# Performance work log

Measured on AMD Instinct MI355X. Metric: run time of the kernel, lower is better.

Reference implementation:

```python
import jax, jax.numpy as jnp
import numpy as np

BS, C, H, W = 64, 3, 512, 512
DROP_PIX = 0.3          # fraction of pixels dropped
NOISE_STD = 0.1         # gaussian multiplicative noise std
RNG_SEED = 42           # internal forward randomness (torch RNG analog)


def setup_inputs() -> dict:
    key = jax.random.key(0)
    x = jax.random.normal(key, (BS, C, H, W), dtype=jnp.float32)
    return {"x": x}


def reference(x):
    bs, c, h, w = x.shape
    hw = h * w
    len_keep = int(hw * (1.0 - DROP_PIX))
    k_mask, k_noise = jax.random.split(jax.random.key(RNG_SEED))

    # Per-sample random permutation of pixel indices, keep first len_keep.
    # argsort of iid uniforms == uniformly random permutation (all bs at once,
    # replacing the Python loop + per-iteration randperm of the original).
    u = jax.random.uniform(k_mask, (bs, hw))
    keep_idx = jnp.argsort(u, axis=1)[:, :len_keep]          # [bs, len_keep]
    mask = jnp.zeros((bs, hw), dtype=x.dtype)
    mask = mask.at[jnp.arange(bs)[:, None], keep_idx].set(1.0)
    mask = mask.reshape(bs, 1, h, w)

    # drop_type == 'zeros'
    x = x * mask

    # additive_noise: gaussian multiplicative noise (real-valued branch)
    noise = jax.random.normal(k_noise, x.shape, dtype=x.dtype) * NOISE_STD + 1.0
    x = x * noise
    return x, mask
```

## Files before the change

### kernel.cpp

```cpp
#include <hip/hip_runtime.h>
#include <hip/hip_bf16.h>

typedef unsigned int u32;
typedef unsigned long long u64;

__host__ __device__ __forceinline__ void tf2x32(u32 k0, u32 k1, u32 x0, u32 x1,
                                                u32& o0, u32& o1)
{
    const u32 ks2 = k0 ^ k1 ^ 0x1BD11BDAu;
    x0 += k0; x1 += k1;
#define TF_R(r) { x0 += x1; x1 = (x1 << (r)) | (x1 >> (32 - (r))); x1 ^= x0; }
    TF_R(13) TF_R(15) TF_R(26) TF_R(6)
    x0 += k1; x1 += ks2 + 1u;
    TF_R(17) TF_R(29) TF_R(16) TF_R(24)
    x0 += ks2; x1 += k0 + 2u;
    TF_R(13) TF_R(15) TF_R(26) TF_R(6)
    x0 += k0; x1 += k1 + 3u;
    TF_R(17) TF_R(29) TF_R(16) TF_R(24)
    x0 += k1; x1 += ks2 + 4u;
    TF_R(13) TF_R(15) TF_R(26) TF_R(6)
    x0 += ks2; x1 += k0 + 5u;
#undef TF_R
    o0 = x0; o1 = x1;
}

__device__ __forceinline__ u32 rbits(u32 k0, u32 k1, u32 e)
{
    u32 o0, o1; tf2x32(k0, k1, 0u, e, o0, o1); return o0 ^ o1;
}

#define HW        262144u
#define PMASK     262143u
#define KEEP      183500u
#define NX        50331648u
#define NM        16777216u
#define LO_F      (-0.99999994039535522461f)

__device__ __forceinline__ float noise_from_bits(u32 bits)
{
    float f  = __uint_as_float((bits >> 9) | 0x3F800000u) - 1.0f;
    float un = fmaf(f, 2.0f, LO_F);
    un = fmaxf(LO_F, un);
    float w = -__logf(fmaf(-un, un, 1.0f));
    float p;
    if (w < 5.0f) {
        w -= 2.5f;
        p = 2.81022636e-08f;
        p = fmaf(p, w, 3.43273939e-07f);
        p = fmaf(p, w, -3.5233877e-06f);
        p = fmaf(p, w, -4.39150654e-06f);
        p = fmaf(p, w, 0.00021858087f);
        p = fmaf(p, w, -0.00125372503f);
        p = fmaf(p, w, -0.00417768164f);
        p = fmaf(p, w, 0.246640727f);
        p = fmaf(p, w, 1.50140941f);
    } else {
        w = __fsqrt_rn(w) - 3.0f;
        p = -0.000200214257f;
        p = fmaf(p, w, 0.000100950558f);
        p = fmaf(p, w, 0.00134934322f);
        p = fmaf(p, w, -0.00367342844f);
        p = fmaf(p, w, 0.00573950773f);
        p = fmaf(p, w, -0.0076224613f);
        p = fmaf(p, w, 0.00943887047f);
        p = fmaf(p, w, 1.00167406f);
        p = fmaf(p, w, 2.83297682f);
    }
    float ei = p * un;
    return fmaf(1.41421356f * ei, 0.1f, 1.0f);
}

__global__ __launch_bounds__(256) void k1_gen_hist(u32 mk0, u32 mk1, u32* mbuf, u32* hist)
{
    __shared__ u32 lh[4096];
    const int t = threadIdx.x;
    const u32 blk = blockIdx.x;
    const u32 row = blk >> 4;
    const u32 base = blk << 14;
#pragma unroll
    for (int i = 0; i < 16; ++i) lh[t + (i << 8)] = 0;
    __syncthreads();
    uint4* mv = (uint4*)mbuf;
#pragma unroll 1
    for (int i = 0; i < 16; ++i) {
        u32 vi = (u32)(i << 8) + (u32)t;
        u32 e = base + (vi << 2);
        uint4 q;
        q.x = rbits(mk0, mk1, e)     >> 9;
        q.y = rbits(mk0, mk1, e + 1) >> 9;
        q.z = rbits(mk0, mk1, e + 2) >> 9;
        q.w = rbits(mk0, mk1, e + 3) >> 9;
        mv[(base >> 2) + vi] = q;
        atomicAdd(&lh[q.x >> 11], 1u);
        atomicAdd(&lh[q.y >> 11], 1u);
        atomicAdd(&lh[q.z >> 11], 1u);
        atomicAdd(&lh[q.w >> 11], 1u);
    }
    __syncthreads();
    u32* gh = hist + (row << 12);
#pragma unroll
    for (int i = 0; i < 16; ++i) {
        u32 idx = (u32)t + (i << 8);
        u32 v = lh[idx];
        if (v) atomicAdd(&gh[idx], v);
    }
}

template <int PER>
__device__ __forceinline__ void rank_scan(const u32* h, u32 k, u32* sh, u32& bin, u32& rem)
{
    const int t = threadIdx.x;
    u32 v[PER]; u32 s = 0;
#pragma unroll
    for (int i = 0; i < PER; ++i) { v[i] = h[t * PER + i]; s += v[i]; }
    sh[t] = s;
    __syncthreads();
    if (t == 0) {
        u32 run = 0; u32 c = 0;
        for (; c < 255u; ++c) { u32 cs = sh[c]; if (run + cs >= k) break; run += cs; }
        sh[256] = c; sh[257] = run;
    }
    __syncthreads();
    u32 c = sh[256];
    if (t == (int)c) {
        u32 run = sh[257];
        u32 b = (u32)t * PER + PER - 1; u32 r = k - run;
#pragma unroll
        for (int i = 0; i < PER; ++i) {
            if (run + v[i] >= k) { b = (u32)t * PER + i; r = k - run; break; }
            run += v[i];
        }
        sh[256] = b; sh[257] = r;
    }
    __syncthreads();
    bin = sh[256]; rem = sh[257];
    __syncthreads();
}

__global__ __launch_bounds__(256) void k2b_finehist(const u32* mbuf, const u32* hist,
                                                    u32* fhist, u32* rowBr)
{
    __shared__ u32 sh[258];
    __shared__ u32 fh[2048];
    const int t = threadIdx.x;
    const u32 blk = blockIdx.x;
    const u32 row = blk >> 4;
    u32 B, r;
    rank_scan<16>(hist + (row << 12), KEEP, sh, B, r);
    if ((blk & 15u) == 0 && t == 0) { rowBr[row * 2] = B; rowBr[row * 2 + 1] = r; }
#pragma unroll
    for (int i = 0; i < 8; ++i) fh[t + (i << 8)] = 0;
    __syncthreads();
    const uint4* mv = (const uint4*)mbuf + (blk << 12);
#pragma unroll 1
    for (int i = 0; i < 16; ++i) {
        uint4 q = mv[(i << 8) + t];
        if ((q.x >> 11) == B) atomicAdd(&fh[q.x & 2047u], 1u);
        if ((q.y >> 11) == B) atomicAdd(&fh[q.y & 2047u], 1u);
        if ((q.z >> 11) == B) atomicAdd(&fh[q.z & 2047u], 1u);
        if ((q.w >> 11) == B) atomicAdd(&fh[q.w & 2047u], 1u);
    }
    __syncthreads();
    u32* gf = fhist + (row << 11);
#pragma unroll
    for (int i = 0; i < 8; ++i) {
        u32 idx = (u32)t + (i << 8);
        u32 v = fh[idx];
        if (v) atomicAdd(&gf[idx], v);
    }
}

__global__ __launch_bounds__(256) void k2d_ties(const u32* mbuf, const u32* fhist,
                                                const u32* rowBr, u32* rowM,
                                                u32* tiecnt, u32* tielist)
{
    __shared__ u32 sh[258];
    const int t = threadIdx.x;
    const u32 blk = blockIdx.x;
    const u32 row = blk >> 4;
    u32 r = rowBr[row * 2 + 1];
    u32 B = rowBr[row * 2];
    u32 f, r2;
    rank_scan<8>(fhist + (row << 11), r, sh, f, r2);
    u32 mstar = (B << 11) | f;
    if ((blk & 15u) == 0 && t == 0) { rowM[row * 2] = mstar; rowM[row * 2 + 1] = r2; }
    const uint4* mv = (const uint4*)mbuf + (blk << 12);
#pragma unroll 1
    for (int i = 0; i < 16; ++i) {
        u32 vi = (u32)(i << 8) + (u32)t;
        uint4 q = mv[vi];
        u32 p = ((blk & 15u) << 14) + (vi << 2);
        if (q.x == mstar) { u32 pos = atomicAdd(&tiecnt[row], 1u); if (pos < 256u) tielist[(row << 8) + pos] = p; }
        if (q.y == mstar) { u32 pos = atomicAdd(&tiecnt[row], 1u); if (pos < 256u) tielist[(row << 8) + pos] = p + 1; }
        if (q.z == mstar) { u32 pos = atomicAdd(&tiecnt[row], 1u); if (pos < 256u) tielist[(row << 8) + pos] = p + 2; }
        if (q.w == mstar) { u32 pos = atomicAdd(&tiecnt[row], 1u); if (pos < 256u) tielist[(row << 8) + pos] = p + 3; }
    }
}

__global__ __launch_bounds__(64) void k2e_select(const u32* rowM, const u32* tiecnt,
                                                 const u32* tielist, u64* rowsel)
{
    __shared__ u32 list[256];
    const int t = threadIdx.x;
    const u32 row = blockIdx.x;
    u32 mstar = rowM[row * 2], r2 = rowM[row * 2 + 1];
    u32 cnt = tiecnt[row]; if (cnt > 256u) cnt = 256u;
    for (u32 i = (u32)t; i < cnt; i += 64u) list[i] = tielist[(row << 8) + i];
    __syncthreads();
    if (t == 0) {
        if (r2 > cnt) r2 = cnt;
        u32 pstar = 0;
        for (u32 it = 0; it < r2; ++it) {
            u32 mn = 0xFFFFFFFFu, mi = 0;
            for (u32 i2 = 0; i2 < cnt; ++i2) if (list[i2] < mn) { mn = list[i2]; mi = i2; }
            pstar = mn; list[mi] = 0xFFFFFFFFu;
        }
        rowsel[row] = ((u64)mstar << 18) | (u64)pstar;
    }
}

__global__ __launch_bounds__(256) void k3_mask(u32* mbuf, const u64* rowsel)
{
    u32 tid = blockIdx.x * 256u + threadIdx.x;
    u32 row = tid >> 16;
    u64 kst = rowsel[row];
    uint4 q = ((const uint4*)mbuf)[tid];
    u32 p = (tid << 2) & PMASK;
    float4 o;
    o.x = ((((u64)q.x << 18) | (u64)(p))     <= kst) ? 1.0f : 0.0f;
    o.y = ((((u64)q.y << 18) | (u64)(p + 1)) <= kst) ? 1.0f : 0.0f;
    o.z = ((((u64)q.z << 18) | (u64)(p + 2)) <= kst) ? 1.0f : 0.0f;
    o.w = ((((u64)q.w << 18) | (u64)(p + 3)) <= kst) ? 1.0f : 0.0f;
    ((float4*)mbuf)[tid] = o;
}

__global__ __launch_bounds__(256) void k4_final(const float4* x4, const float* maskf,
                                                float4* out4, u32 nk0, u32 nk1)
{
    u32 tid = blockIdx.x * 256u + threadIdx.x;
    u32 e = tid << 2;
    u32 b = e / 786432u;
    u32 p = e & PMASK;
    float4 mk = *(const float4*)(maskf + ((b << 18) | p));
    float4 xv = x4[tid];
    float4 r;
    r.x = (xv.x * mk.x) * noise_from_bits(rbits(nk0, nk1, e));
    r.y = (xv.y * mk.y) * noise_from_bits(rbits(nk0, nk1, e + 1));
    r.z = (xv.z * mk.z) * noise_from_bits(rbits(nk0, nk1, e + 2));
    r.w = (xv.w * mk.w) * noise_from_bits(rbits(nk0, nk1, e + 3));
    out4[tid] = r;
}

extern "C" void kernel_launch(void* const* d_in, const int* in_sizes, int n_in,
                              void* d_out, int out_size, void* d_ws, size_t ws_size,
                              hipStream_t stream) {
    const float* x = (const float*)d_in[0];
    float* xout = (float*)d_out;
    u32*  outu = (u32*)d_out;
    u32*  mbuf = (u32*)(xout + NX);

    u32* hist    = outu;
    u32* fhist   = outu + 262144;
    u32* tiecnt  = outu + 393216;
    u32* tielist = outu + 393472;
    u32* rowBr   = outu + 409856;
    u32* rowM    = outu + 410112;
    u64* rowsel  = (u64*)(outu + 410368);

    u32 mk0, mk1, nk0, nk1;
    tf2x32(0u, 42u, 0u, 0u, mk0, mk1);
    tf2x32(0u, 42u, 0u, 1u, nk0, nk1);

    hipMemsetAsync(hist, 0, (262144u + 131072u + 64u) * sizeof(u32), stream);
    k1_gen_hist<<<1024, 256, 0, stream>>>(mk0, mk1, mbuf, hist);
    k2b_finehist<<<1024, 256, 0, stream>>>(mbuf, hist, fhist, rowBr);
    k2d_ties<<<1024, 256, 0, stream>>>(mbuf, fhist, rowBr, rowM, tiecnt, tielist);
    k2e_select<<<64, 64, 0, stream>>>(rowM, tiecnt, tielist, rowsel);
    k3_mask<<<16384, 256, 0, stream>>>(mbuf, rowsel);
    k4_final<<<49152, 256, 0, stream>>>((const float4*)x, (const float*)mbuf,
                                        (float4*)xout, nk0, nk1);
    (void)d_ws; (void)ws_size; (void)in_sizes; (void)n_in; (void)out_size;
}
```

Measured before the change: 514.2 us.

## Replace multi-pass radix select with windowed candidate select and fused mask/noise kernel

The exact multi-pass histogram selection over a stored 64MB key buffer is replaced by a single pass. That pass regenerates the random keys, counts keys below a fixed window near the expected 70% quantile, and collects only in-window candidates per row. A single small kernel per row then finds the exact threshold from those candidates. The final kernel recomputes the mask keys from the RNG and produces the mask and all three noisy channels in one pass. This removes most global memory traffic and several launches, at the cost of hashing the mask keys twice and relying on the threshold statistically falling inside the window (candidate capacity caps).

```diff
diff --git a/kernel.cpp b/kernel.cpp
--- a/kernel.cpp
+++ b/kernel.cpp
@@ -1,8 +1,8 @@
 #include <hip/hip_runtime.h>
-#include <hip/hip_bf16.h>
 
 typedef unsigned int u32;
 typedef unsigned long long u64;
+typedef unsigned char u8;
 
 __host__ __device__ __forceinline__ void tf2x32(u32 k0, u32 k1, u32 x0, u32 x1,
                                                 u32& o0, u32& o1)
@@ -35,6 +35,19 @@
 #define NX        50331648u
 #define NM        16777216u
 #define LO_F      (-0.99999994039535522461f)
+
+#define WLO       5806464u
+#define WWIDTH    131072u
+#define NBIN      4096
+#define ROWCAP    6144
+#define BLKCAP    512
+
+#define CAND_B    (64u * ROWCAP * 8u)
+#define WS_BYTES  (CAND_B + 512u + 512u)
+
+__device__ u64 g_cand[64 * ROWCAP];
+__device__ u64 g_rowsel[64];
+__device__ u32 g_cnts[128];
 
 __device__ __forceinline__ float noise_from_bits(u32 bits)
 {
@@ -70,185 +83,156 @@
     return fmaf(1.41421356f * ei, 0.1f, 1.0f);
 }
 
-__global__ __launch_bounds__(256) void k1_gen_hist(u32 mk0, u32 mk1, u32* mbuf, u32* hist)
-{
-    __shared__ u32 lh[4096];
+__global__ __launch_bounds__(256) void k1_scan(u32 mk0, u32 mk1,
+                                               u32* __restrict__ cnts,
+                                               u64* __restrict__ cand)
+{
+    __shared__ u64 s_cand[BLKCAP];
+    __shared__ u32 s_cnt, s_below, s_base;
     const int t = threadIdx.x;
     const u32 blk = blockIdx.x;
     const u32 row = blk >> 4;
     const u32 base = blk << 14;
-#pragma unroll
-    for (int i = 0; i < 16; ++i) lh[t + (i << 8)] = 0;
-    __syncthreads();
-    uint4* mv = (uint4*)mbuf;
+    if (t == 0) { s_cnt = 0; s_below = 0; }
+    __syncthreads();
+    u32 below = 0;
 #pragma unroll 1
     for (int i = 0; i < 16; ++i) {
         u32 vi = (u32)(i << 8) + (u32)t;
         u32 e = base + (vi << 2);
-        uint4 q;
-        q.x = rbits(mk0, mk1, e)     >> 9;
-        q.y = rbits(mk0, mk1, e + 1) >> 9;
-        q.z = rbits(mk0, mk1, e + 2) >> 9;
-        q.w = rbits(mk0, mk1, e + 3) >> 9;
-        mv[(base >> 2) + vi] = q;
-        atomicAdd(&lh[q.x >> 11], 1u);
-        atomicAdd(&lh[q.y >> 11], 1u);
-        atomicAdd(&lh[q.z >> 11], 1u);
-        atomicAdd(&lh[q.w >> 11], 1u);
-    }
-    __syncthreads();
-    u32* gh = hist + (row << 12);
-#pragma unroll
-    for (int i = 0; i < 16; ++i) {
-        u32 idx = (u32)t + (i << 8);
-        u32 v = lh[idx];
-        if (v) atomicAdd(&gh[idx], v);
-    }
-}
-
-template <int PER>
-__device__ __forceinline__ void rank_scan(const u32* h, u32 k, u32* sh, u32& bin, u32& rem)
-{
+#pragma unroll
+        for (int j = 0; j < 4; ++j) {
+            u32 m = rbits(mk0, mk1, e + (u32)j) >> 9;
+            below += (m < WLO) ? 1u : 0u;
+            if (m - WLO < WWIDTH) {
+                u32 p = ((blk & 15u) << 14) + (vi << 2) + (u32)j;
+                u32 pos = atomicAdd(&s_cnt, 1u);
+                if (pos < BLKCAP) s_cand[pos] = ((u64)m << 18) | (u64)p;
+            }
+        }
+    }
+    atomicAdd(&s_below, below);
+    __syncthreads();
+    u32 cnt = s_cnt; if (cnt > BLKCAP) cnt = BLKCAP;
+    if (t == 0) {
+        atomicAdd(&cnts[row], s_below);
+        s_base = atomicAdd(&cnts[64 + row], cnt);
+    }
+    __syncthreads();
+    u32 gbase = s_base;
+    for (u32 i = (u32)t; i < cnt; i += 256u) {
+        u32 gi = gbase + i;
+        if (gi < ROWCAP) cand[row * ROWCAP + gi] = s_cand[i];
+    }
+}
+
+__global__ __launch_bounds__(256) void k2_select(u32* __restrict__ cnts,
+                                                 const u64* __restrict__ cand,
+                                                 u64* __restrict__ rowsel)
+{
+    __shared__ u32 h[NBIN];
+    __shared__ u32 sh[258];
+    __shared__ u64 tie[64];
+    __shared__ u32 tiecnt;
     const int t = threadIdx.x;
-    u32 v[PER]; u32 s = 0;
-#pragma unroll
-    for (int i = 0; i < PER; ++i) { v[i] = h[t * PER + i]; s += v[i]; }
+    const u32 row = blockIdx.x;
+    u32 n = cnts[64 + row]; if (n > ROWCAP) n = ROWCAP;
+    u32 below = cnts[row];
+    u32 r = KEEP - below;
+#pragma unroll
+    for (int i = 0; i < NBIN / 256; ++i) h[t + (i << 8)] = 0;
+    if (t == 0) tiecnt = 0;
+    __syncthreads();
+    const u64* rc = cand + row * ROWCAP;
+    for (u32 i = (u32)t; i < n; i += 256u) {
+        u32 m = (u32)(rc[i] >> 18);
+        atomicAdd(&h[(m - WLO) >> 5], 1u);
+    }
+    __syncthreads();
+    u32 v[16]; u32 s = 0;
+#pragma unroll
+    for (int i = 0; i < 16; ++i) { v[i] = h[t * 16 + i]; s += v[i]; }
     sh[t] = s;
     __syncthreads();
     if (t == 0) {
         u32 run = 0; u32 c = 0;
-        for (; c < 255u; ++c) { u32 cs = sh[c]; if (run + cs >= k) break; run += cs; }
+        for (; c < 255u; ++c) { u32 cs = sh[c]; if (run + cs >= r) break; run += cs; }
         sh[256] = c; sh[257] = run;
     }
     __syncthreads();
     u32 c = sh[256];
     if (t == (int)c) {
         u32 run = sh[257];
-        u32 b = (u32)t * PER + PER - 1; u32 r = k - run;
-#pragma unroll
-        for (int i = 0; i < PER; ++i) {
-            if (run + v[i] >= k) { b = (u32)t * PER + i; r = k - run; break; }
+        u32 b = (u32)t * 16u + 15u; u32 r2 = r - run;
+#pragma unroll
+        for (int i = 0; i < 16; ++i) {
+            if (run + v[i] >= r) { b = (u32)t * 16u + (u32)i; r2 = r - run; break; }
             run += v[i];
         }
-        sh[256] = b; sh[257] = r;
-    }
-    __syncthreads();
-    bin = sh[256]; rem = sh[257];
-    __syncthreads();
-}
-
-__global__ __launch_bounds__(256) void k2b_finehist(const u32* mbuf, const u32* hist,
-                                                    u32* fhist, u32* rowBr)
-{
-    __shared__ u32 sh[258];
-    __shared__ u32 fh[2048];
-    const int t = threadIdx.x;
-    const u32 blk = blockIdx.x;
-    const u32 row = blk >> 4;
-    u32 B, r;
-    rank_scan<16>(hist + (row << 12), KEEP, sh, B, r);
-    if ((blk & 15u) == 0 && t == 0) { rowBr[row * 2] = B; rowBr[row * 2 + 1] = r; }
-#pragma unroll
-    for (int i = 0; i < 8; ++i) fh[t + (i << 8)] = 0;
-    __syncthreads();
-    const uint4* mv = (const uint4*)mbuf + (blk << 12);
-#pragma unroll 1
-    for (int i = 0; i < 16; ++i) {
-        uint4 q = mv[(i << 8) + t];
-        if ((q.x >> 11) == B) atomicAdd(&fh[q.x & 2047u], 1u);
-        if ((q.y >> 11) == B) atomicAdd(&fh[q.y & 2047u], 1u);
-        if ((q.z >> 11) == B) atomicAdd(&fh[q.z & 2047u], 1u);
-        if ((q.w >> 11) == B) atomicAdd(&fh[q.w & 2047u], 1u);
-    }
-    __syncthreads();
-    u32* gf = fhist + (row << 11);
-#pragma unroll
-    for (int i = 0; i < 8; ++i) {
-        u32 idx = (u32)t + (i << 8);
-        u32 v = fh[idx];
-        if (v) atomicAdd(&gf[idx], v);
-    }
-}
-
-__global__ __launch_bounds__(256) void k2d_ties(const u32* mbuf, const u32* fhist,
-                                                const u32* rowBr, u32* rowM,
-                                                u32* tiecnt, u32* tielist)
-{
-    __shared__ u32 sh[258];
-    const int t = threadIdx.x;
-    const u32 blk = blockIdx.x;
-    const u32 row = blk >> 4;
-    u32 r = rowBr[row * 2 + 1];
-    u32 B = rowBr[row * 2];
-    u32 f, r2;
-    rank_scan<8>(fhist + (row << 11), r, sh, f, r2);
-    u32 mstar = (B << 11) | f;
-    if ((blk & 15u) == 0 && t == 0) { rowM[row * 2] = mstar; rowM[row * 2 + 1] = r2; }
-    const uint4* mv = (const uint4*)mbuf + (blk << 12);
-#pragma unroll 1
-    for (int i = 0; i < 16; ++i) {
-        u32 vi = (u32)(i << 8) + (u32)t;
-        uint4 q = mv[vi];
-        u32 p = ((blk & 15u) << 14) + (vi << 2);
-        if (q.x == mstar) { u32 pos = atomicAdd(&tiecnt[row], 1u); if (pos < 256u) tielist[(row << 8) + pos] = p; }
-        if (q.y == mstar) { u32 pos = atomicAdd(&tiecnt[row], 1u); if (pos < 256u) tielist[(row << 8) + pos] = p + 1; }
-        if (q.z == mstar) { u32 pos = atomicAdd(&tiecnt[row], 1u); if (pos < 256u) tielist[(row << 8) + pos] = p + 2; }
-        if (q.w == mstar) { u32 pos = atomicAdd(&tiecnt[row], 1u); if (pos < 256u) tielist[(row << 8) + pos] = p + 3; }
-    }
-}
-
-__global__ __launch_bounds__(64) void k2e_select(const u32* rowM, const u32* tiecnt,
-                                                 const u32* tielist, u64* rowsel)
-{
-    __shared__ u32 list[256];
-    const int t = threadIdx.x;
-    const u32 row = blockIdx.x;
-    u32 mstar = rowM[row * 2], r2 = rowM[row * 2 + 1];
-    u32 cnt = tiecnt[row]; if (cnt > 256u) cnt = 256u;
-    for (u32 i = (u32)t; i < cnt; i += 64u) list[i] = tielist[(row << 8) + i];
+        sh[256] = b; sh[257] = r2;
+    }
+    __syncthreads();
+    u32 bstar = sh[256], r2 = sh[257];
+    u32 mlo = WLO + (bstar << 5), mhi = mlo + 32u;
+    for (u32 i = (u32)t; i < n; i += 256u) {
+        u64 k = rc[i];
+        u32 m = (u32)(k >> 18);
+        if (m >= mlo && m < mhi) {
+            u32 pos = atomicAdd(&tiecnt, 1u);
+            if (pos < 64u) tie[pos] = k;
+        }
+    }
     __syncthreads();
     if (t == 0) {
+        u32 cnt = tiecnt; if (cnt > 64u) cnt = 64u;
         if (r2 > cnt) r2 = cnt;
-        u32 pstar = 0;
+        u64 kst = 0;
         for (u32 it = 0; it < r2; ++it) {
-            u32 mn = 0xFFFFFFFFu, mi = 0;
-            for (u32 i2 = 0; i2 < cnt; ++i2) if (list[i2] < mn) { mn = list[i2]; mi = i2; }
-            pstar = mn; list[mi] = 0xFFFFFFFFu;
-        }
-        rowsel[row] = ((u64)mstar << 18) | (u64)pstar;
-    }
-}
-
-__global__ __launch_bounds__(256) void k3_mask(u32* mbuf, const u64* rowsel)
+            u64 mn = ~0ull; u32 mi = 0;
+            for (u32 i2 = 0; i2 < cnt; ++i2) if (tie[i2] < mn) { mn = tie[i2]; mi = i2; }
+            kst = mn; tie[mi] = ~0ull;
+        }
+        rowsel[row] = kst;
+        cnts[row] = 0;
+        cnts[64 + row] = 0;
+    }
+}
+
+__global__ __launch_bounds__(256) void k34_final(const float4* __restrict__ x4,
+                                                 float4* __restrict__ out4,
+                                                 float4* __restrict__ mask4,
+                                                 const u64* __restrict__ rowsel,
+                                                 u32 mk0, u32 mk1, u32 nk0, u32 nk1)
 {
     u32 tid = blockIdx.x * 256u + threadIdx.x;
     u32 row = tid >> 16;
     u64 kst = rowsel[row];
-    uint4 q = ((const uint4*)mbuf)[tid];
-    u32 p = (tid << 2) & PMASK;
-    float4 o;
-    o.x = ((((u64)q.x << 18) | (u64)(p))     <= kst) ? 1.0f : 0.0f;
-    o.y = ((((u64)q.y << 18) | (u64)(p + 1)) <= kst) ? 1.0f : 0.0f;
-    o.z = ((((u64)q.z << 18) | (u64)(p + 2)) <= kst) ? 1.0f : 0.0f;
-    o.w = ((((u64)q.w << 18) | (u64)(p + 3)) <= kst) ? 1.0f : 0.0f;
-    ((float4*)mbuf)[tid] = o;
-}
-
-__global__ __launch_bounds__(256) void k4_final(const float4* x4, const float* maskf,
-                                                float4* out4, u32 nk0, u32 nk1)
-{
-    u32 tid = blockIdx.x * 256u + threadIdx.x;
     u32 e = tid << 2;
-    u32 b = e / 786432u;
     u32 p = e & PMASK;
-    float4 mk = *(const float4*)(maskf + ((b << 18) | p));
-    float4 xv = x4[tid];
-    float4 r;
-    r.x = (xv.x * mk.x) * noise_from_bits(rbits(nk0, nk1, e));
-    r.y = (xv.y * mk.y) * noise_from_bits(rbits(nk0, nk1, e + 1));
-    r.z = (xv.z * mk.z) * noise_from_bits(rbits(nk0, nk1, e + 2));
-    r.w = (xv.w * mk.w) * noise_from_bits(rbits(nk0, nk1, e + 3));
-    out4[tid] = r;
+
+    u32 m0 = rbits(mk0, mk1, e)      >> 9;
+    u32 m1 = rbits(mk0, mk1, e + 1u) >> 9;
+    u32 m2 = rbits(mk0, mk1, e + 2u) >> 9;
+    u32 m3 = rbits(mk0, mk1, e + 3u) >> 9;
+    float4 mk;
+    mk.x = ((((u64)m0 << 18) | (u64)(p))      <= kst) ? 1.0f : 0.0f;
+    mk.y = ((((u64)m1 << 18) | (u64)(p + 1u)) <= kst) ? 1.0f : 0.0f;
+    mk.z = ((((u64)m2 << 18) | (u64)(p + 2u)) <= kst) ? 1.0f : 0.0f;
+    mk.w = ((((u64)m3 << 18) | (u64)(p + 3u)) <= kst) ? 1.0f : 0.0f;
+    mask4[tid] = mk;
+
+    u32 b3 = row * 3u;
+#pragma unroll
+    for (u32 cc = 0; cc < 3u; ++cc) {
+        u32 en = ((b3 + cc) << 18) | p;
+        float4 xv = x4[en >> 2];
+        float4 r;
+        r.x = (xv.x * mk.x) * noise_from_bits(rbits(nk0, nk1, en));
+        r.y = (xv.y * mk.y) * noise_from_bits(rbits(nk0, nk1, en + 1u));
+        r.z = (xv.z * mk.z) * noise_from_bits(rbits(nk0, nk1, en + 2u));
+        r.w = (xv.w * mk.w) * noise_from_bits(rbits(nk0, nk1, en + 3u));
+        out4[en >> 2] = r;
+    }
 }
 
 extern "C" void kernel_launch(void* const* d_in, const int* in_sizes, int n_in,
@@ -256,28 +240,29 @@
                               hipStream_t stream) {
     const float* x = (const float*)d_in[0];
     float* xout = (float*)d_out;
-    u32*  outu = (u32*)d_out;
-    u32*  mbuf = (u32*)(xout + NX);
-
-    u32* hist    = outu;
-    u32* fhist   = outu + 262144;
-    u32* tiecnt  = outu + 393216;
-    u32* tielist = outu + 393472;
-    u32* rowBr   = outu + 409856;
-    u32* rowM    = outu + 410112;
-    u64* rowsel  = (u64*)(outu + 410368);
+    float* maskf = xout + NX;
 
     u32 mk0, mk1, nk0, nk1;
     tf2x32(0u, 42u, 0u, 0u, mk0, mk1);
     tf2x32(0u, 42u, 0u, 1u, nk0, nk1);
 
-    hipMemsetAsync(hist, 0, (262144u + 131072u + 64u) * sizeof(u32), stream);
-    k1_gen_hist<<<1024, 256, 0, stream>>>(mk0, mk1, mbuf, hist);
-    k2b_finehist<<<1024, 256, 0, stream>>>(mbuf, hist, fhist, rowBr);
-    k2d_ties<<<1024, 256, 0, stream>>>(mbuf, fhist, rowBr, rowM, tiecnt, tielist);
-    k2e_select<<<64, 64, 0, stream>>>(rowM, tiecnt, tielist, rowsel);
-    k3_mask<<<16384, 256, 0, stream>>>(mbuf, rowsel);
-    k4_final<<<49152, 256, 0, stream>>>((const float4*)x, (const float*)mbuf,
-                                        (float4*)xout, nk0, nk1);
-    (void)d_ws; (void)ws_size; (void)in_sizes; (void)n_in; (void)out_size;
-}
+    u64* cand; u64* rowsel; u32* cnts;
+    if (d_ws != nullptr && ws_size >= (size_t)WS_BYTES) {
+        u8* w = (u8*)d_ws;
+        cand   = (u64*)w;
+        rowsel = (u64*)(w + CAND_B);
+        cnts   = (u32*)(w + CAND_B + 512u);
+        hipMemsetAsync(cnts, 0, 512u, stream);
+    } else {
+        hipGetSymbolAddress((void**)&cand,   HIP_SYMBOL(g_cand));
+        hipGetSymbolAddress((void**)&rowsel, HIP_SYMBOL(g_rowsel));
+        hipGetSymbolAddress((void**)&cnts,   HIP_SYMBOL(g_cnts));
+    }
+
+    k1_scan<<<1024, 256, 0, stream>>>(mk0, mk1, cnts, cand);
+    k2_select<<<64, 256, 0, stream>>>(cnts, cand, rowsel);
+    k34_final<<<16384, 256, 0, stream>>>((const float4*)x, (float4*)xout,
+                                         (float4*)maskf, rowsel,
+                                         mk0, mk1, nk0, nk1);
+    (void)in_sizes; (void)n_in; (void)out_size;
+}
```

New measurement: 493.3 us. -4.1%, faster.
